# Kernel optimization log

Measured on AMD Instinct MI355X. Metric: run time of the kernel, lower is better.

## Reference

```python
import jax, jax.numpy as jnp
import numpy as np

N_NODES = 100000
N_EDGES = 800000
D_IN = 128
D_H = 512


def _glorot(key, shape):
    fan_in, fan_out = shape[1], shape[0]
    lim = jnp.sqrt(6.0 / (fan_in + fan_out))
    return jax.random.uniform(key, shape, jnp.float32, -lim, lim)


def setup_inputs() -> dict:
    key = jax.random.key(0)
    ks = jax.random.split(key, 16)
    x = jax.random.normal(ks[0], (N_NODES, D_IN), jnp.float32)
    edge_index = jax.random.randint(ks[1], (2, N_EDGES), 0, N_NODES, jnp.int64)
    return {
        "x": x,
        "edge_index": edge_index,
        # SAGEConv layer1: lin_l (neighbors, with bias), lin_r (root, no bias)
        "Wl1": _glorot(ks[2], (D_H, D_IN)), "bl1": jnp.zeros((D_H,), jnp.float32),
        "Wr1": _glorot(ks[3], (D_H, D_IN)),
        # SAGEConv layer2
        "Wl2": _glorot(ks[4], (D_H, D_H)), "bl2": jnp.zeros((D_H,), jnp.float32),
        "Wr2": _glorot(ks[5], (D_H, D_H)),
        # SAGEConv layer3
        "Wl3": _glorot(ks[6], (D_H, D_H)), "bl3": jnp.zeros((D_H,), jnp.float32),
        "Wr3": _glorot(ks[7], (D_H, D_H)),
        # residual projections W, W2 (nn.Linear with bias)
        "Ww": _glorot(ks[8], (D_H, D_IN)), "bw": jnp.zeros((D_H,), jnp.float32),
        "Ww2": _glorot(ks[9], (D_H, D_IN)), "bw2": jnp.zeros((D_H,), jnp.float32),
        # shared PReLU parameter (nn.PReLU default: single param init 0.25)
        "a": jnp.array(0.25, jnp.float32),
    }


def _prelu(x, a):
    return jnp.where(x > 0, x, a * x)


def _sage_conv(x, src, dst, Wl, bl, Wr):
    # mean-aggregate neighbor features x[src] onto dst, then linear + root term
    msg = jax.ops.segment_sum(x[src], dst, num_segments=N_NODES)  # [N, d]
    deg = jax.ops.segment_sum(jnp.ones((src.shape[0],), x.dtype), dst,
                              num_segments=N_NODES)
    agg = msg / jnp.maximum(deg, 1.0)[:, None]
    return agg @ Wl.T + bl + x @ Wr.T


def reference(x, edge_index, Wl1, bl1, Wr1, Wl2, bl2, Wr2, Wl3, bl3, Wr3,
              Ww, bw, Ww2, bw2, a):
    src, dst = edge_index[0], edge_index[1]
    h1 = _prelu(_sage_conv(x, src, dst, Wl1, bl1, Wr1), a)
    h2 = _prelu(_sage_conv(h1 + (x @ Ww.T + bw), src, dst, Wl2, bl2, Wr2), a)
    h3 = _prelu(_sage_conv(h2 + h1 + (x @ Ww2.T + bw2), src, dst, Wl3, bl3, Wr3), a)
    return h3
```

## Files before the change

kernel.cpp:

```cpp
#include <hip/hip_runtime.h>
#include <stddef.h>

#define NN 100000
#define NE 800000
#define DIN 128
#define DH 512
#define MT 782

typedef __attribute__((ext_vector_type(8))) short sh8;
typedef __attribute__((ext_vector_type(4))) float f32x4;

__device__ __forceinline__ unsigned short f2b(float f) {
  unsigned u = __float_as_uint(f);
  return (unsigned short)((u + 0x7FFFu + ((u >> 16) & 1u)) >> 16);
}
__device__ __forceinline__ float b2f(unsigned short s) {
  return __uint_as_float(((unsigned)s) << 16);
}

__device__ __forceinline__ void gload16(const unsigned short* g, unsigned short* l) {
  __builtin_amdgcn_global_load_lds(
      (const __attribute__((address_space(1))) void*)g,
      (__attribute__((address_space(3))) void*)l, 16, 0, 0);
}


__global__ void k_count(const int* __restrict__ dst, int* __restrict__ cnt) {
  int i = blockIdx.x * blockDim.x + threadIdx.x;
  if (i < NE) atomicAdd(&cnt[dst[i]], 1);
}

__global__ void k_invdeg(const int* __restrict__ cnt, float* __restrict__ inv_deg) {
  int i = blockIdx.x * blockDim.x + threadIdx.x;
  if (i < NN) inv_deg[i] = 1.0f / (float)(cnt[i] > 1 ? cnt[i] : 1);
}

__global__ void k_scan1(const int* __restrict__ cnt, int* __restrict__ excl,
                        int* __restrict__ partials) {
  __shared__ int sh[256];
  int tid = threadIdx.x;
  int base = blockIdx.x * 1024 + tid * 4;
  int v[4]; int s = 0;
#pragma unroll
  for (int i = 0; i < 4; i++) { int idx = base + i; v[i] = (idx < NN) ? cnt[idx] : 0; s += v[i]; }
  sh[tid] = s; __syncthreads();
  for (int off = 1; off < 256; off <<= 1) {
    int t = (tid >= off) ? sh[tid - off] : 0;
    __syncthreads();
    sh[tid] += t;
    __syncthreads();
  }
  int run = sh[tid] - s;
#pragma unroll
  for (int i = 0; i < 4; i++) { int idx = base + i; if (idx < NN) excl[idx] = run; run += v[i]; }
  if (tid == 255) partials[blockIdx.x] = sh[255];
}

__global__ void k_scan2(int* __restrict__ partials, int* __restrict__ row_start, int nparts) {
  __shared__ int sh[128];
  int tid = threadIdx.x;
  int v = (tid < nparts) ? partials[tid] : 0;
  sh[tid] = v; __syncthreads();
  for (int off = 1; off < 128; off <<= 1) {
    int t = (tid >= off) ? sh[tid - off] : 0;
    __syncthreads();
    sh[tid] += t;
    __syncthreads();
  }
  if (tid < nparts) partials[tid] = sh[tid] - v;
  if (tid == 127) row_start[NN] = sh[127];
}

__global__ void k_scan3(int* __restrict__ excl, const int* __restrict__ partials) {
  int i = blockIdx.x * blockDim.x + threadIdx.x;
  if (i < NN) excl[i] += partials[i >> 10];
}

__global__ void k_fill(const int* __restrict__ src, const int* __restrict__ dst,
                       const int* __restrict__ row_start, int* __restrict__ cursor,
                       int* __restrict__ ssrc) {
  int i = blockIdx.x * blockDim.x + threadIdx.x;
  if (i < NE) {
    int d = dst[i];
    int pos = atomicAdd(&cursor[d], 1);
    ssrc[row_start[d] + pos] = src[i];
  }
}


__global__ void k_f2b(const float* __restrict__ src, unsigned short* __restrict__ dst, int n) {
  int i = (blockIdx.x * blockDim.x + threadIdx.x) * 4;
  if (i < n) {
    float4 v = *(const float4*)(src + i);
    ushort4 o;
    o.x = f2b(v.x); o.y = f2b(v.y); o.z = f2b(v.z); o.w = f2b(v.w);
    *(ushort4*)(dst + i) = o;
  }
}


__global__ __launch_bounds__(256) void k_aggb512(
    const unsigned short* __restrict__ z, const int* __restrict__ rs,
    const int* __restrict__ ssrc, const float* __restrict__ inv_deg,
    unsigned short* __restrict__ agg) {
  int w = (blockIdx.x * blockDim.x + threadIdx.x) >> 6;
  int lane = threadIdx.x & 63;
  if (w >= NN) return;
  int e0 = rs[w], e1 = rs[w + 1];
  float acc[8] = {0, 0, 0, 0, 0, 0, 0, 0};
  for (int e = e0; e < e1; ++e) {
    int s = ssrc[e];
    sh8 v = *(const sh8*)(z + (size_t)s * DH + lane * 8);
#pragma unroll
    for (int j = 0; j < 8; ++j) acc[j] += b2f((unsigned short)v[j]);
  }
  float s0 = inv_deg[w];
  sh8 o;
#pragma unroll
  for (int j = 0; j < 8; ++j) o[j] = (short)f2b(acc[j] * s0);
  *(sh8*)(agg + (size_t)w * DH + lane * 8) = o;
}

__global__ __launch_bounds__(256) void k_aggb128(
    const unsigned short* __restrict__ z, const int* __restrict__ rs,
    const int* __restrict__ ssrc, const float* __restrict__ inv_deg,
    unsigned short* __restrict__ agg) {
  int w = (blockIdx.x * blockDim.x + threadIdx.x) >> 6;
  int lane = threadIdx.x & 63;
  if (w >= NN) return;
  int e0 = rs[w], e1 = rs[w + 1];
  float a0 = 0.f, a1 = 0.f;
  for (int e = e0; e < e1; ++e) {
    int s = ssrc[e];
    unsigned v = *(const unsigned*)(z + (size_t)s * DIN + lane * 2);
    a0 += b2f((unsigned short)(v & 0xFFFFu));
    a1 += b2f((unsigned short)(v >> 16));
  }
  float s0 = inv_deg[w];
  unsigned o = (unsigned)f2b(a0 * s0) | ((unsigned)f2b(a1 * s0) << 16);
  *(unsigned*)(agg + (size_t)w * DIN + lane * 2) = o;
}


__device__ __forceinline__ void stage_tile(
    unsigned short* ldsA, unsigned short* ldsB,
    const unsigned short* __restrict__ A, int sA, int m0,
    const unsigned short* __restrict__ B, int sB, int n0,
    int k0, int tid) {
  const int w = tid >> 6, l = tid & 63;
  const int kc = (l & 3) * 8;
  const int rsub = l >> 2;
#pragma unroll
  for (int i = 0; i < 2; ++i) {
    int rl = w * 32 + i * 16 + rsub;
    int ra = m0 + rl; if (ra >= NN) ra = NN - 1;
    gload16(A + (size_t)ra * sA + k0 + kc, ldsA + (size_t)(w * 32 + i * 16) * 32);
    gload16(B + (size_t)(n0 + rl) * sB + k0 + kc, ldsB + (size_t)(w * 32 + i * 16) * 32);
  }
}

__device__ __forceinline__ void mfma_step(
    const unsigned short* As, const unsigned short* Bs,
    int wr, int wc, int r16, int kg, f32x4 (&acc)[4][4]) {
  sh8 af[4], bf[4];
#pragma unroll
  for (int i = 0; i < 4; ++i)
    af[i] = *(const sh8*)&As[(wr + i * 16 + r16) * 32 + kg * 8];
#pragma unroll
  for (int j = 0; j < 4; ++j)
    bf[j] = *(const sh8*)&Bs[(wc + j * 16 + r16) * 32 + kg * 8];
#pragma unroll
  for (int i = 0; i < 4; ++i)
#pragma unroll
    for (int j = 0; j < 4; ++j)
      acc[i][j] = __builtin_amdgcn_mfma_f32_16x16x32_bf16(af[i], bf[j], acc[i][j], 0, 0, 0);
}

__global__ __launch_bounds__(256, 2) void k_gemm1(
    const unsigned short* __restrict__ ag, const unsigned short* __restrict__ xb,
    const unsigned short* __restrict__ Wl1, const unsigned short* __restrict__ Wr1,
    const unsigned short* __restrict__ Ww, const unsigned short* __restrict__ Ww2,
    const float* __restrict__ bl1, const float* __restrict__ bw,
    const float* __restrict__ bw2, const float* __restrict__ aptr,
    unsigned short* __restrict__ z2o, unsigned short* __restrict__ z3po) {
  __shared__ __align__(16) unsigned short As[2][128 * 32];
  __shared__ __align__(16) unsigned short Bs[2][128 * 32];
  const int tid = threadIdx.x;
  const int m0 = blockIdx.x * 128, n0 = blockIdx.y * 128;
  const int wid = tid >> 6, lane = tid & 63;
  const int r16 = lane & 15, kg = lane >> 4;
  const int wr = (wid >> 1) * 64, wc = (wid & 1) * 64;

  f32x4 a0[4][4], a1[4][4], a2[4][4];
#pragma unroll
  for (int i = 0; i < 4; ++i)
#pragma unroll
    for (int j = 0; j < 4; ++j) { a0[i][j] = 0.f; a1[i][j] = 0.f; a2[i][j] = 0.f; }

  auto stage = [&](int s, int buf) {
    const int seg = s >> 2, k0 = (s & 3) * 32;
    const unsigned short* Ap = (seg == 0) ? ag : xb;
    const unsigned short* Bp = (seg == 0) ? Wl1 : (seg == 1) ? Wr1 : (seg == 2) ? Ww : Ww2;
    stage_tile(As[buf], Bs[buf], Ap, DIN, m0, Bp, DIN, n0, k0, tid);
  };

  stage(0, 0);
  __syncthreads();
  int cur = 0;
  for (int s = 0; s < 16; ++s) {
    if (s + 1 < 16) stage(s + 1, cur ^ 1);
    const int seg = s >> 2;
    if (seg <= 1)      mfma_step(As[cur], Bs[cur], wr, wc, r16, kg, a0);
    else if (seg == 2) mfma_step(As[cur], Bs[cur], wr, wc, r16, kg, a1);
    else               mfma_step(As[cur], Bs[cur], wr, wc, r16, kg, a2);
    __syncthreads();
    cur ^= 1;
  }

  const float aval = aptr[0];
#pragma unroll
  for (int i = 0; i < 4; ++i) {
    const int mbase = m0 + wr + i * 16 + kg * 4;
#pragma unroll
    for (int j = 0; j < 4; ++j) {
      const int col = n0 + wc + j * 16 + r16;
      const float b1 = bl1[col], b2 = bw[col], b3 = bw2[col];
#pragma unroll
      for (int r = 0; r < 4; ++r) {
        const int m = mbase + r;
        if (m >= NN) continue;
        float h1 = a0[i][j][r] + b1;
        h1 = h1 > 0.f ? h1 : aval * h1;
        z2o[(size_t)m * DH + col] = f2b(h1 + a1[i][j][r] + b2);
        z3po[(size_t)m * DH + col] = f2b(h1 + a2[i][j][r] + b3);
      }
    }
  }
}

template <bool LAST>
__global__ __launch_bounds__(256, 4) void k_gemm23(
    const unsigned short* __restrict__ Aag, const unsigned short* __restrict__ Az,
    const unsigned short* __restrict__ Wl, const unsigned short* __restrict__ Wr,
    const float* __restrict__ bl, const float* __restrict__ aptr,
    const unsigned short* __restrict__ z3p, void* __restrict__ outp) {
  __shared__ __align__(16) unsigned short As[2][128 * 32];
  __shared__ __align__(16) unsigned short Bs[2][128 * 32];
  const int tid = threadIdx.x;
  const int m0 = blockIdx.x * 128, n0 = blockIdx.y * 128;
  const int wid = tid >> 6, lane = tid & 63;
  const int r16 = lane & 15, kg = lane >> 4;
  const int wr = (wid >> 1) * 64, wc = (wid & 1) * 64;

  f32x4 acc[4][4];
#pragma unroll
  for (int i = 0; i < 4; ++i)
#pragma unroll
    for (int j = 0; j < 4; ++j) acc[i][j] = 0.f;

  auto stage = [&](int s, int buf) {
    const int k0 = (s & 15) * 32;
    const unsigned short* Ap = (s < 16) ? Aag : Az;
    const unsigned short* Bp = (s < 16) ? Wl : Wr;
    stage_tile(As[buf], Bs[buf], Ap, DH, m0, Bp, DH, n0, k0, tid);
  };

  stage(0, 0);
  __syncthreads();
  int cur = 0;
  for (int s = 0; s < 32; ++s) {
    if (s + 1 < 32) stage(s + 1, cur ^ 1);
    mfma_step(As[cur], Bs[cur], wr, wc, r16, kg, acc);
    __syncthreads();
    cur ^= 1;
  }

  const float aval = aptr[0];
  float* outf = (float*)outp;
  unsigned short* outb = (unsigned short*)outp;
#pragma unroll
  for (int i = 0; i < 4; ++i) {
    const int mbase = m0 + wr + i * 16 + kg * 4;
#pragma unroll
    for (int j = 0; j < 4; ++j) {
      const int col = n0 + wc + j * 16 + r16;
      const float bv = bl[col];
#pragma unroll
      for (int r = 0; r < 4; ++r) {
        const int m = mbase + r;
        if (m >= NN) continue;
        float h = acc[i][j][r] + bv;
        h = h > 0.f ? h : aval * h;
        if constexpr (LAST) {
          outf[(size_t)m * DH + col] = h;
        } else {
          outb[(size_t)m * DH + col] = f2b(h + b2f(z3p[(size_t)m * DH + col]));
        }
      }
    }
  }
}


extern "C" void kernel_launch(void* const* d_in, const int* in_sizes, int n_in,
                              void* d_out, int out_size, void* d_ws, size_t ws_size,
                              hipStream_t stream) {
  const float* x = (const float*)d_in[0];
  const int* ei = (const int*)d_in[1];
  const float* Wl1 = (const float*)d_in[2];
  const float* bl1 = (const float*)d_in[3];
  const float* Wr1 = (const float*)d_in[4];
  const float* Wl2 = (const float*)d_in[5];
  const float* bl2 = (const float*)d_in[6];
  const float* Wr2 = (const float*)d_in[7];
  const float* Wl3 = (const float*)d_in[8];
  const float* bl3 = (const float*)d_in[9];
  const float* Wr3 = (const float*)d_in[10];
  const float* Ww  = (const float*)d_in[11];
  const float* bw  = (const float*)d_in[12];
  const float* Ww2 = (const float*)d_in[13];
  const float* bw2 = (const float*)d_in[14];
  const float* ap  = (const float*)d_in[15];
  float* out = (float*)d_out;

  const size_t MP = 100096;
  char* w = (char*)d_ws;
  size_t off = 0;
  unsigned short* xb   = (unsigned short*)(w + off); off += MP * DIN * 2;
  unsigned short* ag1  = (unsigned short*)(w + off); off += MP * DIN * 2;
  unsigned short* agb  = (unsigned short*)(w + off); off += MP * DH * 2;
  unsigned short* zb   = (unsigned short*)(w + off); off += MP * DH * 2;
  unsigned short* zc   = (unsigned short*)(w + off); off += MP * DH * 2;
  unsigned short* z3pb = (unsigned short*)(w + off); off += MP * DH * 2;
  unsigned short* Wl1b = (unsigned short*)(w + off); off += (size_t)DH * DIN * 2;
  unsigned short* Wr1b = (unsigned short*)(w + off); off += (size_t)DH * DIN * 2;
  unsigned short* Wwb  = (unsigned short*)(w + off); off += (size_t)DH * DIN * 2;
  unsigned short* Ww2b = (unsigned short*)(w + off); off += (size_t)DH * DIN * 2;
  unsigned short* Wl2b = (unsigned short*)(w + off); off += (size_t)DH * DH * 2;
  unsigned short* Wr2b = (unsigned short*)(w + off); off += (size_t)DH * DH * 2;
  unsigned short* Wl3b = (unsigned short*)(w + off); off += (size_t)DH * DH * 2;
  unsigned short* Wr3b = (unsigned short*)(w + off); off += (size_t)DH * DH * 2;
  float* inv_deg = (float*)(w + off); off += (size_t)NN * 4;
  int* row_start = (int*)(w + off); off += (size_t)(NN + 1) * 4;
  int* cursor = (int*)(w + off); off += (size_t)NN * 4;
  int* ssrc = (int*)(w + off); off += (size_t)NE * 4;
  int* partials = (int*)(w + off); off += 512;

  const int* esrc = ei;
  const int* edst = ei + NE;

  hipMemsetAsync(cursor, 0, NN * 4, stream);
  k_count<<<(NE + 255) / 256, 256, 0, stream>>>(edst, cursor);
  k_invdeg<<<(NN + 255) / 256, 256, 0, stream>>>(cursor, inv_deg);
  k_scan1<<<(NN + 1023) / 1024, 256, 0, stream>>>(cursor, row_start, partials);
  k_scan2<<<1, 128, 0, stream>>>(partials, row_start, (NN + 1023) / 1024);
  k_scan3<<<(NN + 255) / 256, 256, 0, stream>>>(row_start, partials);
  hipMemsetAsync(cursor, 0, NN * 4, stream);
  k_fill<<<(NE + 255) / 256, 256, 0, stream>>>(esrc, edst, row_start, cursor, ssrc);

  const int WK = DH * DIN;
  const int WB = DH * DH;
  k_f2b<<<(WK / 4 + 255) / 256, 256, 0, stream>>>(Wl1, Wl1b, WK);
  k_f2b<<<(WK / 4 + 255) / 256, 256, 0, stream>>>(Wr1, Wr1b, WK);
  k_f2b<<<(WK / 4 + 255) / 256, 256, 0, stream>>>(Ww,  Wwb,  WK);
  k_f2b<<<(WK / 4 + 255) / 256, 256, 0, stream>>>(Ww2, Ww2b, WK);
  k_f2b<<<(WB / 4 + 255) / 256, 256, 0, stream>>>(Wl2, Wl2b, WB);
  k_f2b<<<(WB / 4 + 255) / 256, 256, 0, stream>>>(Wr2, Wr2b, WB);
  k_f2b<<<(WB / 4 + 255) / 256, 256, 0, stream>>>(Wl3, Wl3b, WB);
  k_f2b<<<(WB / 4 + 255) / 256, 256, 0, stream>>>(Wr3, Wr3b, WB);
  k_f2b<<<(NN * DIN / 4 + 255) / 256, 256, 0, stream>>>(x, xb, NN * DIN);

  dim3 gg(MT, 4);

  k_aggb128<<<(NN + 3) / 4, 256, 0, stream>>>(xb, row_start, ssrc, inv_deg, ag1);
  k_gemm1<<<gg, 256, 0, stream>>>(ag1, xb, Wl1b, Wr1b, Wwb, Ww2b, bl1, bw, bw2, ap,
                                  zb, z3pb);
  k_aggb512<<<(NN + 3) / 4, 256, 0, stream>>>(zb, row_start, ssrc, inv_deg, agb);
  k_gemm23<false><<<gg, 256, 0, stream>>>(agb, zb, Wl2b, Wr2b, bl2, ap, z3pb, zc);
  k_aggb512<<<(NN + 3) / 4, 256, 0, stream>>>(zc, row_start, ssrc, inv_deg, agb);
  k_gemm23<true><<<gg, 256, 0, stream>>>(agb, zc, Wl3b, Wr3b, bl3, ap, nullptr, out);
}
```

Before: 1.078 ms.

## Triple-buffer GEMM pipeline with vmcnt waits, XCD-aware block remap, unrolled gathers

The GEMM kernels move from double to triple LDS buffering. They prefetch two stages ahead, wait with explicit s_waitcnt vmcnt counts and raw barriers instead of __syncthreads, and raise wave priority around the MFMA section. The launch grid becomes 1D, and block ids are remapped so consecutive tiles land on the same XCD, aiming for better L2 reuse. The aggregation kernels process two edges per iteration to expose more memory-level parallelism. The cost is more LDS per block and a lower occupancy bound for gemm23. The hand-coded vmcnt counts must match the number of loads issued per stage, or the pipeline will read incomplete tiles.

```diff
diff --git a/kernel.cpp b/kernel.cpp
--- a/kernel.cpp
+++ b/kernel.cpp
@@ -6,6 +6,8 @@
 #define DIN 128
 #define DH 512
 #define MT 782
+#define NWG (MT * 4)
+#define CPX (NWG / 8)
 
 typedef __attribute__((ext_vector_type(8))) short sh8;
 typedef __attribute__((ext_vector_type(4))) float f32x4;
@@ -23,6 +25,9 @@
       (const __attribute__((address_space(1))) void*)g,
       (__attribute__((address_space(3))) void*)l, 16, 0, 0);
 }
+
+#define SCHED_FENCE() __builtin_amdgcn_sched_barrier(0)
+#define VMCNT(n) asm volatile("s_waitcnt vmcnt(" #n ")" ::: "memory")
 
 
 __global__ void k_count(const int* __restrict__ dst, int* __restrict__ cnt) {
@@ -108,11 +113,19 @@
   if (w >= NN) return;
   int e0 = rs[w], e1 = rs[w + 1];
   float acc[8] = {0, 0, 0, 0, 0, 0, 0, 0};
-  for (int e = e0; e < e1; ++e) {
-    int s = ssrc[e];
-    sh8 v = *(const sh8*)(z + (size_t)s * DH + lane * 8);
-#pragma unroll
-    for (int j = 0; j < 8; ++j) acc[j] += b2f((unsigned short)v[j]);
+  int e = e0;
+  for (; e + 1 < e1; e += 2) {
+    int sa = ssrc[e], sb = ssrc[e + 1];
+    sh8 va = *(const sh8*)(z + (size_t)sa * DH + lane * 8);
+    sh8 vb = *(const sh8*)(z + (size_t)sb * DH + lane * 8);
+#pragma unroll
+    for (int j = 0; j < 8; ++j) acc[j] += b2f((unsigned short)va[j]) + b2f((unsigned short)vb[j]);
+  }
+  if (e < e1) {
+    int sa = ssrc[e];
+    sh8 va = *(const sh8*)(z + (size_t)sa * DH + lane * 8);
+#pragma unroll
+    for (int j = 0; j < 8; ++j) acc[j] += b2f((unsigned short)va[j]);
   }
   float s0 = inv_deg[w];
   sh8 o;
@@ -130,11 +143,18 @@
   if (w >= NN) return;
   int e0 = rs[w], e1 = rs[w + 1];
   float a0 = 0.f, a1 = 0.f;
-  for (int e = e0; e < e1; ++e) {
-    int s = ssrc[e];
-    unsigned v = *(const unsigned*)(z + (size_t)s * DIN + lane * 2);
-    a0 += b2f((unsigned short)(v & 0xFFFFu));
-    a1 += b2f((unsigned short)(v >> 16));
+  int e = e0;
+  for (; e + 1 < e1; e += 2) {
+    int sa = ssrc[e], sb = ssrc[e + 1];
+    unsigned va = *(const unsigned*)(z + (size_t)sa * DIN + lane * 2);
+    unsigned vb = *(const unsigned*)(z + (size_t)sb * DIN + lane * 2);
+    a0 += b2f((unsigned short)(va & 0xFFFFu)) + b2f((unsigned short)(vb & 0xFFFFu));
+    a1 += b2f((unsigned short)(va >> 16)) + b2f((unsigned short)(vb >> 16));
+  }
+  if (e < e1) {
+    unsigned va = *(const unsigned*)(z + (size_t)ssrc[e] * DIN + lane * 2);
+    a0 += b2f((unsigned short)(va & 0xFFFFu));
+    a1 += b2f((unsigned short)(va >> 16));
   }
   float s0 = inv_deg[w];
   unsigned o = (unsigned)f2b(a0 * s0) | ((unsigned)f2b(a1 * s0) << 16);
@@ -176,6 +196,23 @@
       acc[i][j] = __builtin_amdgcn_mfma_f32_16x16x32_bf16(af[i], bf[j], acc[i][j], 0, 0, 0);
 }
 
+#define PIPE_WAIT(s, S)                 \
+  do {                                  \
+    if ((s) < (S) - 2) VMCNT(8);        \
+    else if ((s) == (S) - 2) VMCNT(4);  \
+    else VMCNT(0);                      \
+    SCHED_FENCE();                      \
+    __builtin_amdgcn_s_barrier();       \
+    SCHED_FENCE();                      \
+  } while (0)
+
+#define PIPE_END()                      \
+  do {                                  \
+    SCHED_FENCE();                      \
+    __builtin_amdgcn_s_barrier();       \
+    SCHED_FENCE();                      \
+  } while (0)
+
 __global__ __launch_bounds__(256, 2) void k_gemm1(
     const unsigned short* __restrict__ ag, const unsigned short* __restrict__ xb,
     const unsigned short* __restrict__ Wl1, const unsigned short* __restrict__ Wr1,
@@ -183,10 +220,12 @@
     const float* __restrict__ bl1, const float* __restrict__ bw,
     const float* __restrict__ bw2, const float* __restrict__ aptr,
     unsigned short* __restrict__ z2o, unsigned short* __restrict__ z3po) {
-  __shared__ __align__(16) unsigned short As[2][128 * 32];
-  __shared__ __align__(16) unsigned short Bs[2][128 * 32];
+  __shared__ __align__(16) unsigned short As[3][128 * 32];
+  __shared__ __align__(16) unsigned short Bs[3][128 * 32];
   const int tid = threadIdx.x;
-  const int m0 = blockIdx.x * 128, n0 = blockIdx.y * 128;
+  const int b = blockIdx.x;
+  const int L = (b & 7) * CPX + (b >> 3);
+  const int m0 = (L >> 2) * 128, n0 = (L & 3) * 128;
   const int wid = tid >> 6, lane = tid & 63;
   const int r16 = lane & 15, kg = lane >> 4;
   const int wr = (wid >> 1) * 64, wc = (wid & 1) * 64;
@@ -205,16 +244,20 @@
   };
 
   stage(0, 0);
-  __syncthreads();
-  int cur = 0;
+  stage(1, 1);
+  int cur = 0, nxt = 2;
   for (int s = 0; s < 16; ++s) {
-    if (s + 1 < 16) stage(s + 1, cur ^ 1);
+    if (s + 2 < 16) stage(s + 2, nxt);
+    PIPE_WAIT(s, 16);
     const int seg = s >> 2;
+    __builtin_amdgcn_s_setprio(1);
     if (seg <= 1)      mfma_step(As[cur], Bs[cur], wr, wc, r16, kg, a0);
     else if (seg == 2) mfma_step(As[cur], Bs[cur], wr, wc, r16, kg, a1);
     else               mfma_step(As[cur], Bs[cur], wr, wc, r16, kg, a2);
-    __syncthreads();
-    cur ^= 1;
+    __builtin_amdgcn_s_setprio(0);
+    PIPE_END();
+    cur = (cur == 2) ? 0 : cur + 1;
+    nxt = (nxt == 2) ? 0 : nxt + 1;
   }
 
   const float aval = aptr[0];
@@ -239,15 +282,17 @@
 }
 
 template <bool LAST>
-__global__ __launch_bounds__(256, 4) void k_gemm23(
+__global__ __launch_bounds__(256, 3) void k_gemm23(
     const unsigned short* __restrict__ Aag, const unsigned short* __restrict__ Az,
     const unsigned short* __restrict__ Wl, const unsigned short* __restrict__ Wr,
     const float* __restrict__ bl, const float* __restrict__ aptr,
     const unsigned short* __restrict__ z3p, void* __restrict__ outp) {
-  __shared__ __align__(16) unsigned short As[2][128 * 32];
-  __shared__ __align__(16) unsigned short Bs[2][128 * 32];
+  __shared__ __align__(16) unsigned short As[3][128 * 32];
+  __shared__ __align__(16) unsigned short Bs[3][128 * 32];
   const int tid = threadIdx.x;
-  const int m0 = blockIdx.x * 128, n0 = blockIdx.y * 128;
+  const int b = blockIdx.x;
+  const int L = (b & 7) * CPX + (b >> 3);
+  const int m0 = (L >> 2) * 128, n0 = (L & 3) * 128;
   const int wid = tid >> 6, lane = tid & 63;
   const int r16 = lane & 15, kg = lane >> 4;
   const int wr = (wid >> 1) * 64, wc = (wid & 1) * 64;
@@ -266,13 +311,17 @@
   };
 
   stage(0, 0);
-  __syncthreads();
-  int cur = 0;
+  stage(1, 1);
+  int cur = 0, nxt = 2;
   for (int s = 0; s < 32; ++s) {
-    if (s + 1 < 32) stage(s + 1, cur ^ 1);
+    if (s + 2 < 32) stage(s + 2, nxt);
+    PIPE_WAIT(s, 32);
+    __builtin_amdgcn_s_setprio(1);
     mfma_step(As[cur], Bs[cur], wr, wc, r16, kg, acc);
-    __syncthreads();
-    cur ^= 1;
+    __builtin_amdgcn_s_setprio(0);
+    PIPE_END();
+    cur = (cur == 2) ? 0 : cur + 1;
+    nxt = (nxt == 2) ? 0 : nxt + 1;
   }
 
   const float aval = aptr[0];
@@ -370,13 +419,11 @@
   k_f2b<<<(WB / 4 + 255) / 256, 256, 0, stream>>>(Wr3, Wr3b, WB);
   k_f2b<<<(NN * DIN / 4 + 255) / 256, 256, 0, stream>>>(x, xb, NN * DIN);
 
-  dim3 gg(MT, 4);
-
   k_aggb128<<<(NN + 3) / 4, 256, 0, stream>>>(xb, row_start, ssrc, inv_deg, ag1);
-  k_gemm1<<<gg, 256, 0, stream>>>(ag1, xb, Wl1b, Wr1b, Wwb, Ww2b, bl1, bw, bw2, ap,
-                                  zb, z3pb);
+  k_gemm1<<<NWG, 256, 0, stream>>>(ag1, xb, Wl1b, Wr1b, Wwb, Ww2b, bl1, bw, bw2, ap,
+                                   zb, z3pb);
   k_aggb512<<<(NN + 3) / 4, 256, 0, stream>>>(zb, row_start, ssrc, inv_deg, agb);
-  k_gemm23<false><<<gg, 256, 0, stream>>>(agb, zb, Wl2b, Wr2b, bl2, ap, z3pb, zc);
+  k_gemm23<false><<<NWG, 256, 0, stream>>>(agb, zb, Wl2b, Wr2b, bl2, ap, z3pb, zc);
   k_aggb512<<<(NN + 3) / 4, 256, 0, stream>>>(zc, row_start, ssrc, inv_deg, agb);
-  k_gemm23<true><<<gg, 256, 0, stream>>>(agb, zc, Wl3b, Wr3b, bl3, ap, nullptr, out);
-}
+  k_gemm23<true><<<NWG, 256, 0, stream>>>(agb, zc, Wl3b, Wr3b, bl3, ap, nullptr, out);
+}
```

New measurement: 1.005 ms. 1.07x faster.
